# Kernel tuning notes

Measured on AMD Instinct MI355X. Metric: run time of the kernel, lower is better.

## Reference

```python
import jax, jax.numpy as jnp
import numpy as np
from jax.ops import segment_sum, segment_max

N_NODES = 100000
N_EDGES = 1600000
IN, HID, OUT = 256, 64, 40
NEG_SLOPE = 0.2  # DGL GATConv default


def setup_inputs() -> dict:
    key = jax.random.key(0)
    ks = jax.random.split(key, 12)
    feat = jax.random.normal(ks[0], (N_NODES, IN), dtype=jnp.float32)
    src = jax.random.randint(ks[1], (N_EDGES,), 0, N_NODES)
    dst = jax.random.randint(ks[2], (N_EDGES,), 0, N_NODES)
    def xavier(k, shape):
        fan = sum(shape)
        return jax.random.normal(k, shape, dtype=jnp.float32) * jnp.sqrt(2.0 / fan)
    return {
        "feat": feat, "src": src, "dst": dst,
        "W1": xavier(ks[3], (IN, HID)),  "b1": jnp.zeros((HID,), jnp.float32),
        "al1": xavier(ks[4], (HID,)),    "ar1": xavier(ks[5], (HID,)),
        "W2": xavier(ks[6], (HID, OUT)), "b2": jnp.zeros((OUT,), jnp.float32),
        "al2": xavier(ks[7], (OUT,)),    "ar2": xavier(ks[8], (OUT,)),
    }


def gat_layer(x, W, b, attn_l, attn_r, src, dst, n):
    # z: [N, F_out] projected features
    z = x @ W
    el = z @ attn_l          # [N] source attention logits
    er = z @ attn_r          # [N] destination attention logits
    e = jax.nn.leaky_relu(el[src] + er[dst], NEG_SLOPE)  # [E]
    # segment (per-destination) softmax over incoming edges
    m = segment_max(e, dst, num_segments=n)              # [N]
    w = jnp.exp(e - m[dst])                              # [E]
    s = segment_sum(w, dst, num_segments=n)              # [N]
    alpha = w / s[dst]                                   # [E]
    # scatter-add aggregation of alpha * z[src]
    out = segment_sum(alpha[:, None] * z[src], dst, num_segments=n)
    return out + b


def reference(feat, src, dst, W1, b1, al1, ar1, W2, b2, al2, ar2):
    n = feat.shape[0]
    h = gat_layer(feat, W1, b1, al1, ar1, src, dst, n)
    h = jax.nn.relu(h)  # dropout is identity in eval mode
    h = gat_layer(h, W2, b2, al2, ar2, src, dst, n)
    return jax.nn.log_softmax(h, axis=-1)  # [N, out_size]
```

## Files before the change

### kernel.cpp

```cpp
#include <hip/hip_runtime.h>
#include <math.h>

constexpr int NN   = 100000;
constexpr int NE   = 1600000;
constexpr int FIN  = 256;
constexpr int HID  = 64;
constexpr int FOUT = 40;
constexpr float SLOPE = 0.2f;
constexpr int NB    = (NN + 255) / 256;
constexpr int NBUCK = NB;
constexpr int TILE_A = 2048;
constexpr int NWG_A = (NE + TILE_A - 1) / TILE_A;
constexpr int AK = 264;

typedef short  short8  __attribute__((ext_vector_type(8)));
typedef float  floatx4 __attribute__((ext_vector_type(4)));

__device__ inline unsigned short f2bf(float x) {
    union { float f; unsigned int u; } c; c.f = x;
    unsigned int u = c.u;
    return (unsigned short)((u + 0x7FFF + ((u >> 16) & 1)) >> 16);
}

__device__ inline float readlane_f(float v, int l) {
    return __int_as_float(__builtin_amdgcn_readlane(__float_as_int(v), l));
}

__global__ __launch_bounds__(256) void w1t_kernel(
    const float* __restrict__ W1, unsigned short* __restrict__ W1T,
    const float* __restrict__ W2, const float* __restrict__ al2,
    const float* __restrict__ ar2,
    float* __restrict__ wl2, float* __restrict__ wr2)
{
    int idx = blockIdx.x * 256 + threadIdx.x;
    if (idx < FIN * HID) {
        int k = idx >> 6, n = idx & 63;
        W1T[n * FIN + k] = f2bf(W1[idx]);
    }
    if (blockIdx.x == 0 && threadIdx.x < HID) {
        int k = threadIdx.x;
        float a = 0.f, b = 0.f;
        #pragma unroll 8
        for (int j = 0; j < FOUT; ++j) {
            float wv = W2[k * FOUT + j];
            a += wv * al2[j]; b += wv * ar2[j];
        }
        wl2[k] = a; wr2[k] = b;
    }
}

__global__ __launch_bounds__(256) void gemm1_kernel(
    const float* __restrict__ feat, const unsigned short* __restrict__ W1T,
    const float* __restrict__ al, const float* __restrict__ ar,
    const int* __restrict__ dst, int* __restrict__ bcnt,
    _Float16* __restrict__ z, float* __restrict__ el, float* __restrict__ er)
{
    __shared__ unsigned short sBT[64 * AK];
    __shared__ int hist[NBUCK];
    const int t = threadIdx.x;
    const int ntile = blockIdx.x * 64;

    for (int i = t; i < NBUCK; i += 256) hist[i] = 0;
    #pragma unroll
    for (int i = 0; i < 8; ++i) {
        int g = t + 256 * i;
        int row = g >> 5, c8 = g & 31;
        *(uint4*)&sBT[row * AK + 8 * c8] = *(const uint4*)&W1T[row * FIN + 8 * c8];
    }
    __syncthreads();

    {
        int base = (blockIdx.x * 256 + t) * 4;
        if (base < NE) {
            const int4 d4 = *(const int4*)&dst[base];
            atomicAdd(&hist[d4.x >> 8], 1); atomicAdd(&hist[d4.y >> 8], 1);
            atomicAdd(&hist[d4.z >> 8], 1); atomicAdd(&hist[d4.w >> 8], 1);
        }
    }
    __syncthreads();
    for (int i = t; i < NBUCK; i += 256) {
        int hv = hist[i];
        if (hv) atomicAdd(&bcnt[i], hv);
    }

    const int w  = t >> 6;
    const int l  = t & 63;
    const int lr = l & 15;
    const int q  = l >> 4;
    const int m0 = 16 * w;

    int n = ntile + m0 + lr; if (n >= NN) n = NN - 1;
    const float* __restrict__ arow = feat + (size_t)n * FIN;

    floatx4 acc[4];
    #pragma unroll
    for (int tile = 0; tile < 4; ++tile) acc[tile] = 0.f;

    #pragma unroll
    for (int kc = 0; kc < 8; ++kc) {
        const int koff = kc * 32 + 8 * q;
        const float4 fa = *(const float4*)(arow + koff);
        const float4 fb = *(const float4*)(arow + koff + 4);
        short8 av;
        av[0] = (short)f2bf(fa.x); av[1] = (short)f2bf(fa.y);
        av[2] = (short)f2bf(fa.z); av[3] = (short)f2bf(fa.w);
        av[4] = (short)f2bf(fb.x); av[5] = (short)f2bf(fb.y);
        av[6] = (short)f2bf(fb.z); av[7] = (short)f2bf(fb.w);
        #pragma unroll
        for (int tile = 0; tile < 4; ++tile) {
            const short8 bv = *(const short8*)(sBT + (16 * tile + lr) * AK + koff);
            acc[tile] = __builtin_amdgcn_mfma_f32_16x16x32_bf16(av, bv, acc[tile], 0, 0, 0);
        }
    }

    float aln[4], arn[4];
    #pragma unroll
    for (int tile = 0; tile < 4; ++tile) {
        aln[tile] = al[16 * tile + lr];
        arn[tile] = ar[16 * tile + lr];
    }
    #pragma unroll
    for (int r = 0; r < 4; ++r) {
        int mg = ntile + m0 + 4 * q + r;
        float pl = 0.f, pr = 0.f;
        #pragma unroll
        for (int tile = 0; tile < 4; ++tile) {
            float zv = acc[tile][r];
            pl += zv * aln[tile]; pr += zv * arn[tile];
        }
        #pragma unroll
        for (int off = 8; off >= 1; off >>= 1) {
            pl += __shfl_xor(pl, off);
            pr += __shfl_xor(pr, off);
        }
        if (mg < NN) {
            #pragma unroll
            for (int tile = 0; tile < 4; ++tile)
                z[(size_t)mg * HID + 16 * tile + lr] = (_Float16)acc[tile][r];
            if (lr == 0) { el[mg] = pl; er[mg] = pr; }
        }
    }
}

__global__ __launch_bounds__(512) void scan_top_kernel(
    const int* __restrict__ bcnt, int* __restrict__ bofs, int* __restrict__ gcur)
{
    __shared__ int tmp[512];
    int t = threadIdx.x;
    int v = (t < NB) ? bcnt[t] : 0;
    tmp[t] = v; __syncthreads();
    for (int off = 1; off < 512; off <<= 1) {
        int x = (t >= off) ? tmp[t - off] : 0;
        __syncthreads();
        tmp[t] += x;
        __syncthreads();
    }
    int excl = tmp[t] - v;
    if (t < NB) { bofs[t] = excl; gcur[t] = excl; }
    if (t == NB - 1) bofs[NB] = excl + v;
}

__global__ __launch_bounds__(1024) void partitionA_kernel(
    const int* __restrict__ src, const int* __restrict__ dst,
    int* __restrict__ gcur, int* __restrict__ ebuck)
{
    __shared__ int hist[NBUCK];
    __shared__ int lcur[NBUCK];
    const int t = threadIdx.x;
    const int e0 = blockIdx.x * TILE_A;
    const int e1 = (e0 + TILE_A < NE) ? e0 + TILE_A : NE;

    for (int i = t; i < NBUCK; i += 1024) hist[i] = 0;
    __syncthreads();
    for (int e = e0 + t; e < e1; e += 1024)
        atomicAdd(&hist[dst[e] >> 8], 1);
    __syncthreads();
    for (int i = t; i < NBUCK; i += 1024) {
        int hv = hist[i];
        lcur[i] = hv ? atomicAdd(&gcur[i], hv) : 0;
    }
    __syncthreads();
    for (int e = e0 + t; e < e1; e += 1024) {
        int d = dst[e], s = src[e];
        int p = atomicAdd(&lcur[d >> 8], 1);
        ebuck[p] = (s << 8) | (d & 255);
    }
}

__global__ __launch_bounds__(1024) void partitionB_kernel(
    const int* __restrict__ bofs, const int* __restrict__ ebuck,
    int* __restrict__ row_ptr, int* __restrict__ esrc)
{
    __shared__ int sdeg[256];
    __shared__ int sscan[256];
    __shared__ int scur[256];
    const int b = blockIdx.x;
    const int n0 = b << 8;
    const int t = threadIdx.x;
    const int r0 = bofs[b], r1 = bofs[b + 1];

    if (t < 256) sdeg[t] = 0;
    __syncthreads();
    for (int e = r0 + t; e < r1; e += 1024)
        atomicAdd(&sdeg[ebuck[e] & 255], 1);
    __syncthreads();

    if (t < 256) sscan[t] = sdeg[t];
    __syncthreads();
    for (int off = 1; off < 256; off <<= 1) {
        int x = 0;
        if (t < 256 && t >= off) x = sscan[t - off];
        __syncthreads();
        if (t < 256) sscan[t] += x;
        __syncthreads();
    }
    if (t < 256) {
        int excl = sscan[t] - sdeg[t];
        if (n0 + t < NN) row_ptr[n0 + t] = r0 + excl;
        scur[t] = r0 + excl;
    }
    if (b == NBUCK - 1 && t == 0) row_ptr[NN] = NE;
    __syncthreads();

    for (int e = r0 + t; e < r1; e += 1024) {
        int pk = ebuck[e];
        int p = atomicAdd(&scur[pk & 255], 1);
        esrc[p] = pk >> 8;
    }
}

template<bool FIRST>
__global__ __launch_bounds__(256) void gat_gather_kernel(
    const int* __restrict__ row_ptr, const int* __restrict__ esrc,
    const float* __restrict__ el, const float* __restrict__ er,
    const _Float16* __restrict__ zin, const float* __restrict__ b1,
    const float* __restrict__ wl2, const float* __restrict__ wr2,
    _Float16* __restrict__ hout, float* __restrict__ haggout,
    float* __restrict__ el2, float* __restrict__ er2)
{
    const int w = threadIdx.x >> 6, lane = threadIdx.x & 63;
    const int d = blockIdx.x * 4 + w;
    const int r0 = row_ptr[d], r1 = row_ptr[d + 1];
    const int cnt = r1 - r0;
    const float erd = er[d];

    float accv = 0.f;
    float s = 0.f;

    if (cnt <= 64) {
        int sn = 0; float v = -INFINITY;
        if (lane < cnt) {
            sn = esrc[r0 + lane];
            v = el[sn] + erd;
            v = (v >= 0.f) ? v : SLOPE * v;
        }
        float m = v;
        #pragma unroll
        for (int off = 32; off >= 1; off >>= 1) m = fmaxf(m, __shfl_xor(m, off));
        float wv = (lane < cnt) ? __expf(v - m) : 0.f;
        s = wv;
        #pragma unroll
        for (int off = 32; off >= 1; off >>= 1) s += __shfl_xor(s, off);
        {
            int j = 0;
            for (; j + 8 <= cnt; j += 8) {
                float a0 = 0.f, a1 = 0.f;
                #pragma unroll
                for (int qq = 0; qq < 8; qq += 2) {
                    float w0 = readlane_f(wv, j + qq);
                    int   s0 = __builtin_amdgcn_readlane(sn, j + qq);
                    float w1 = readlane_f(wv, j + qq + 1);
                    int   s1 = __builtin_amdgcn_readlane(sn, j + qq + 1);
                    a0 += w0 * (float)zin[(size_t)s0 * HID + lane];
                    a1 += w1 * (float)zin[(size_t)s1 * HID + lane];
                }
                accv += a0 + a1;
            }
            for (; j < cnt; ++j) {
                float w0 = readlane_f(wv, j);
                int   s0 = __builtin_amdgcn_readlane(sn, j);
                accv += w0 * (float)zin[(size_t)s0 * HID + lane];
            }
        }
    } else {
        float m = -INFINITY;
        for (int e = r0 + lane; e < r1; e += 64) {
            float v = el[esrc[e]] + erd;
            v = (v >= 0.f) ? v : SLOPE * v;
            m = fmaxf(m, v);
        }
        #pragma unroll
        for (int off = 32; off >= 1; off >>= 1) m = fmaxf(m, __shfl_xor(m, off));
        for (int base = r0; base < r1; base += 64) {
            int e = base + lane;
            float wv = 0.f; int sn = 0;
            if (e < r1) {
                sn = esrc[e];
                float v = el[sn] + erd;
                v = (v >= 0.f) ? v : SLOPE * v;
                wv = __expf(v - m);
            }
            s += wv;
            int c = r1 - base; if (c > 64) c = 64;
            {
                int j = 0;
                for (; j + 4 <= c; j += 4) {
                    float a0 = 0.f, a1 = 0.f;
                    #pragma unroll
                    for (int qq = 0; qq < 4; qq += 2) {
                        float w0 = readlane_f(wv, j + qq);
                        int   s0 = __builtin_amdgcn_readlane(sn, j + qq);
                        float w1 = readlane_f(wv, j + qq + 1);
                        int   s1 = __builtin_amdgcn_readlane(sn, j + qq + 1);
                        a0 += w0 * (float)zin[(size_t)s0 * HID + lane];
                        a1 += w1 * (float)zin[(size_t)s1 * HID + lane];
                    }
                    accv += a0 + a1;
                }
                for (; j < c; ++j) {
                    float w0 = readlane_f(wv, j);
                    int   s0 = __builtin_amdgcn_readlane(sn, j);
                    accv += w0 * (float)zin[(size_t)s0 * HID + lane];
                }
            }
        }
        #pragma unroll
        for (int off = 32; off >= 1; off >>= 1) s += __shfl_xor(s, off);
    }

    float res = (cnt > 0) ? (accv / s) : 0.f;

    if (FIRST) {
        float hval = res + b1[lane];
        hval = (hval > 0.f) ? hval : 0.f;
        hout[(size_t)d * HID + lane] = (_Float16)hval;
        float pl = hval * wl2[lane];
        float pr = hval * wr2[lane];
        #pragma unroll
        for (int off = 32; off >= 1; off >>= 1) {
            pl += __shfl_xor(pl, off); pr += __shfl_xor(pr, off);
        }
        if (lane == 0) { el2[d] = pl; er2[d] = pr; }
    } else {
        haggout[(size_t)d * HID + lane] = res;
    }
}

__global__ __launch_bounds__(256) void out_kernel(
    const float* __restrict__ hagg, const float* __restrict__ W2,
    const float* __restrict__ b2, float* __restrict__ out)
{
    __shared__ float sh[4][64];
    const int w = threadIdx.x >> 6, lane = threadIdx.x & 63;
    const int n = blockIdx.x * 4 + w;
    sh[w][lane] = hagg[(size_t)n * HID + lane];
    __syncthreads();
    float acc = 0.f;
    if (lane < FOUT) {
        #pragma unroll 8
        for (int k = 0; k < HID; ++k) acc += sh[w][k] * W2[k * FOUT + lane];
    }
    float v = (lane < FOUT) ? acc + b2[lane] : -INFINITY;
    float mx = v;
    #pragma unroll
    for (int off = 32; off >= 1; off >>= 1) mx = fmaxf(mx, __shfl_xor(mx, off));
    float ex = (lane < FOUT) ? __expf(v - mx) : 0.f;
    float sm = ex;
    #pragma unroll
    for (int off = 32; off >= 1; off >>= 1) sm += __shfl_xor(sm, off);
    if (lane < FOUT) out[(size_t)n * FOUT + lane] = v - mx - __logf(sm);
}

extern "C" void kernel_launch(void* const* d_in, const int* in_sizes, int n_in,
                              void* d_out, int out_size, void* d_ws, size_t ws_size,
                              hipStream_t stream) {
    const float* feat = (const float*)d_in[0];
    const int*   src  = (const int*)d_in[1];
    const int*   dst  = (const int*)d_in[2];
    const float* W1   = (const float*)d_in[3];
    const float* b1   = (const float*)d_in[4];
    const float* al1  = (const float*)d_in[5];
    const float* ar1  = (const float*)d_in[6];
    const float* W2   = (const float*)d_in[7];
    const float* b2   = (const float*)d_in[8];
    const float* al2  = (const float*)d_in[9];
    const float* ar2  = (const float*)d_in[10];
    float* out = (float*)d_out;

    char* p = (char*)d_ws;
    float*    hagg = (float*)p;
    _Float16* z1   = (_Float16*)p;  p += (size_t)NN * HID * 4;
    _Float16* h    = (_Float16*)p;  p += (size_t)NN * HID * 2;
    float* el1   = (float*)p;     p += (size_t)NN * 4;
    float* er1   = (float*)p;     p += (size_t)NN * 4;
    float* el2   = (float*)p;     p += (size_t)NN * 4;
    float* er2   = (float*)p;     p += (size_t)NN * 4;
    float* wl2   = (float*)p;     p += HID * 4;
    float* wr2   = (float*)p;     p += HID * 4;
    int*   bcnt  = (int*)p;       p += NB * 4;
    int*   bofs  = (int*)p;       p += (NB + 1) * 4;
    int*   gcur  = (int*)p;       p += NBUCK * 4;
    int*   rowp  = (int*)p;       p += (NN + 1) * 4;
    int*   esrc  = (int*)p;       p += (size_t)NE * 4;
    int*   ebuck = (int*)p;       p += (size_t)NE * 4;
    unsigned short* w1t = (unsigned short*)p;

    hipMemsetAsync(bcnt, 0, NB * sizeof(int), stream);

    w1t_kernel<<<(FIN * HID + 255) / 256, 256, 0, stream>>>(
        W1, w1t, W2, al2, ar2, wl2, wr2);
    gemm1_kernel<<<(NN + 63) / 64, 256, 0, stream>>>(feat, w1t, al1, ar1, dst, bcnt, z1, el1, er1);

    scan_top_kernel<<<1, 512, 0, stream>>>(bcnt, bofs, gcur);
    partitionA_kernel<<<NWG_A, 1024, 0, stream>>>(src, dst, gcur, ebuck);
    partitionB_kernel<<<NBUCK, 1024, 0, stream>>>(bofs, ebuck, rowp, esrc);

    gat_gather_kernel<true><<<NN / 4, 256, 0, stream>>>(
        rowp, esrc, el1, er1, z1, b1, wl2, wr2, h, nullptr, el2, er2);

    gat_gather_kernel<false><<<NN / 4, 256, 0, stream>>>(
        rowp, esrc, el2, er2, h, nullptr, nullptr, nullptr,
        nullptr, hagg, nullptr, nullptr);

    out_kernel<<<NN / 4, 256, 0, stream>>>(hagg, W2, b2, out);
}
```

Baseline: 418.3 us.

## Merge histogram, GEMM and edge partition into fewer kernels with finer buckets

The dst-bucket histogram moves into the weight-prep kernel. The GEMM1 blocks and the partition-A blocks now share one launch, so the projection and the edge bucketing run concurrently. Each partition block recomputes the bucket prefix scan locally, which removes the standalone scan kernel. Buckets shrink from 256 to 128 nodes and the partition kernels use 256-thread blocks, trading redundant per-block scans and more buckets for fewer launches and better overlap.

Result: no change. 410.7 us (-1.8%).

```diff
diff --git a/kernel.cpp b/kernel.cpp
--- a/kernel.cpp
+++ b/kernel.cpp
@@ -7,11 +7,14 @@
 constexpr int HID  = 64;
 constexpr int FOUT = 40;
 constexpr float SLOPE = 0.2f;
-constexpr int NB    = (NN + 255) / 256;
-constexpr int NBUCK = NB;
+constexpr int NBUCK = (NN + 127) / 128;
 constexpr int TILE_A = 2048;
 constexpr int NWG_A = (NE + TILE_A - 1) / TILE_A;
+constexpr int NT_GEMM = (NN + 63) / 64;
 constexpr int AK = 264;
+constexpr int HB = 64;
+constexpr int HIST_EPB = 4096;
+constexpr int NWG_H = (NE + HIST_EPB - 1) / HIST_EPB;
 
 typedef short  short8  __attribute__((ext_vector_type(8)));
 typedef float  floatx4 __attribute__((ext_vector_type(4)));
@@ -26,195 +29,215 @@
     return __int_as_float(__builtin_amdgcn_readlane(__float_as_int(v), l));
 }
 
-__global__ __launch_bounds__(256) void w1t_kernel(
+__device__ inline void scan_buckets(const int* __restrict__ gcnt,
+                                    int* __restrict__ bofs,
+                                    int* __restrict__ tsum, int t)
+{
+    int i0 = 4 * t;
+    int c0 = (i0 + 0 < NBUCK) ? gcnt[i0 + 0] : 0;
+    int c1 = (i0 + 1 < NBUCK) ? gcnt[i0 + 1] : 0;
+    int c2 = (i0 + 2 < NBUCK) ? gcnt[i0 + 2] : 0;
+    int c3 = (i0 + 3 < NBUCK) ? gcnt[i0 + 3] : 0;
+    int s = c0 + c1 + c2 + c3;
+    tsum[t] = s;
+    __syncthreads();
+    for (int off = 1; off < 256; off <<= 1) {
+        int x = (t >= off) ? tsum[t - off] : 0;
+        __syncthreads();
+        tsum[t] += x;
+        __syncthreads();
+    }
+    int e0 = tsum[t] - s;
+    if (i0 + 0 <= NBUCK) bofs[i0 + 0] = e0;
+    if (i0 + 1 <= NBUCK) bofs[i0 + 1] = e0 + c0;
+    if (i0 + 2 <= NBUCK) bofs[i0 + 2] = e0 + c0 + c1;
+    if (i0 + 3 <= NBUCK) bofs[i0 + 3] = e0 + c0 + c1 + c2;
+    __syncthreads();
+}
+
+__global__ __launch_bounds__(256) void prep_kernel(
     const float* __restrict__ W1, unsigned short* __restrict__ W1T,
     const float* __restrict__ W2, const float* __restrict__ al2,
     const float* __restrict__ ar2,
-    float* __restrict__ wl2, float* __restrict__ wr2)
-{
-    int idx = blockIdx.x * 256 + threadIdx.x;
-    if (idx < FIN * HID) {
-        int k = idx >> 6, n = idx & 63;
-        W1T[n * FIN + k] = f2bf(W1[idx]);
-    }
-    if (blockIdx.x == 0 && threadIdx.x < HID) {
-        int k = threadIdx.x;
-        float a = 0.f, b = 0.f;
-        #pragma unroll 8
-        for (int j = 0; j < FOUT; ++j) {
-            float wv = W2[k * FOUT + j];
-            a += wv * al2[j]; b += wv * ar2[j];
-        }
-        wl2[k] = a; wr2[k] = b;
-    }
-}
-
-__global__ __launch_bounds__(256) void gemm1_kernel(
+    float* __restrict__ wl2, float* __restrict__ wr2,
+    const int* __restrict__ dst, int* __restrict__ bcnt)
+{
+    const int t = threadIdx.x;
+    if (blockIdx.x < HB) {
+        int idx = blockIdx.x * 256 + t;
+        if (idx < FIN * HID) {
+            int k = idx >> 6, n = idx & 63;
+            W1T[n * FIN + k] = f2bf(W1[idx]);
+        }
+        if (blockIdx.x == 0 && t < HID) {
+            int k = t;
+            float a = 0.f, b = 0.f;
+            #pragma unroll 8
+            for (int j = 0; j < FOUT; ++j) {
+                float wv = W2[k * FOUT + j];
+                a += wv * al2[j]; b += wv * ar2[j];
+            }
+            wl2[k] = a; wr2[k] = b;
+        }
+    } else {
+        __shared__ int hist[NBUCK];
+        for (int i = t; i < NBUCK; i += 256) hist[i] = 0;
+        __syncthreads();
+        int base = (blockIdx.x - HB) * HIST_EPB + t * 16;
+        #pragma unroll
+        for (int k = 0; k < 4; ++k) {
+            int idx = base + 4 * k;
+            if (idx < NE) {
+                const int4 d4 = *(const int4*)&dst[idx];
+                atomicAdd(&hist[d4.x >> 7], 1); atomicAdd(&hist[d4.y >> 7], 1);
+                atomicAdd(&hist[d4.z >> 7], 1); atomicAdd(&hist[d4.w >> 7], 1);
+            }
+        }
+        __syncthreads();
+        for (int i = t; i < NBUCK; i += 256) {
+            int hv = hist[i];
+            if (hv) atomicAdd(&bcnt[i], hv);
+        }
+    }
+}
+
+__global__ __launch_bounds__(256) void mega_kernel(
     const float* __restrict__ feat, const unsigned short* __restrict__ W1T,
     const float* __restrict__ al, const float* __restrict__ ar,
-    const int* __restrict__ dst, int* __restrict__ bcnt,
+    const int* __restrict__ src, const int* __restrict__ dst,
+    const int* __restrict__ bcnt, int* __restrict__ cur0,
+    int* __restrict__ ebuck,
     _Float16* __restrict__ z, float* __restrict__ el, float* __restrict__ er)
 {
-    __shared__ unsigned short sBT[64 * AK];
-    __shared__ int hist[NBUCK];
+    __shared__ int smem4[8448];
     const int t = threadIdx.x;
-    const int ntile = blockIdx.x * 64;
-
-    for (int i = t; i < NBUCK; i += 256) hist[i] = 0;
-    #pragma unroll
-    for (int i = 0; i < 8; ++i) {
-        int g = t + 256 * i;
-        int row = g >> 5, c8 = g & 31;
-        *(uint4*)&sBT[row * AK + 8 * c8] = *(const uint4*)&W1T[row * FIN + 8 * c8];
-    }
-    __syncthreads();
-
-    {
-        int base = (blockIdx.x * 256 + t) * 4;
-        if (base < NE) {
-            const int4 d4 = *(const int4*)&dst[base];
-            atomicAdd(&hist[d4.x >> 8], 1); atomicAdd(&hist[d4.y >> 8], 1);
-            atomicAdd(&hist[d4.z >> 8], 1); atomicAdd(&hist[d4.w >> 8], 1);
-        }
-    }
-    __syncthreads();
-    for (int i = t; i < NBUCK; i += 256) {
-        int hv = hist[i];
-        if (hv) atomicAdd(&bcnt[i], hv);
-    }
-
-    const int w  = t >> 6;
-    const int l  = t & 63;
-    const int lr = l & 15;
-    const int q  = l >> 4;
-    const int m0 = 16 * w;
-
-    int n = ntile + m0 + lr; if (n >= NN) n = NN - 1;
-    const float* __restrict__ arow = feat + (size_t)n * FIN;
-
-    floatx4 acc[4];
-    #pragma unroll
-    for (int tile = 0; tile < 4; ++tile) acc[tile] = 0.f;
-
-    #pragma unroll
-    for (int kc = 0; kc < 8; ++kc) {
-        const int koff = kc * 32 + 8 * q;
-        const float4 fa = *(const float4*)(arow + koff);
-        const float4 fb = *(const float4*)(arow + koff + 4);
-        short8 av;
-        av[0] = (short)f2bf(fa.x); av[1] = (short)f2bf(fa.y);
-        av[2] = (short)f2bf(fa.z); av[3] = (short)f2bf(fa.w);
-        av[4] = (short)f2bf(fb.x); av[5] = (short)f2bf(fb.y);
-        av[6] = (short)f2bf(fb.z); av[7] = (short)f2bf(fb.w);
+
+    if (blockIdx.x < NT_GEMM) {
+        unsigned short* sBT = (unsigned short*)smem4;
+        const int ntile = blockIdx.x * 64;
+
+        #pragma unroll
+        for (int i = 0; i < 8; ++i) {
+            int g = t + 256 * i;
+            int row = g >> 5, c8 = g & 31;
+            *(uint4*)&sBT[row * AK + 8 * c8] = *(const uint4*)&W1T[row * FIN + 8 * c8];
+        }
+        __syncthreads();
+
+        const int w  = t >> 6;
+        const int l  = t & 63;
+        const int lr = l & 15;
+        const int q  = l >> 4;
+        const int m0 = 16 * w;
+
+        int n = ntile + m0 + lr; if (n >= NN) n = NN - 1;
+        const float* __restrict__ arow = feat + (size_t)n * FIN;
+
+        floatx4 acc[4];
+        #pragma unroll
+        for (int tile = 0; tile < 4; ++tile) acc[tile] = 0.f;
+
+        #pragma unroll
+        for (int kc = 0; kc < 8; ++kc) {
+            const int koff = kc * 32 + 8 * q;
+            const float4 fa = *(const float4*)(arow + koff);
+            const float4 fb = *(const float4*)(arow + koff + 4);
+            short8 av;
+            av[0] = (short)f2bf(fa.x); av[1] = (short)f2bf(fa.y);
+            av[2] = (short)f2bf(fa.z); av[3] = (short)f2bf(fa.w);
+            av[4] = (short)f2bf(fb.x); av[5] = (short)f2bf(fb.y);
+            av[6] = (short)f2bf(fb.z); av[7] = (short)f2bf(fb.w);
+            #pragma unroll
+            for (int tile = 0; tile < 4; ++tile) {
+                const short8 bv = *(const short8*)(sBT + (16 * tile + lr) * AK + koff);
+                acc[tile] = __builtin_amdgcn_mfma_f32_16x16x32_bf16(av, bv, acc[tile], 0, 0, 0);
+            }
+        }
+
+        float aln[4], arn[4];
         #pragma unroll
         for (int tile = 0; tile < 4; ++tile) {
-            const short8 bv = *(const short8*)(sBT + (16 * tile + lr) * AK + koff);
-            acc[tile] = __builtin_amdgcn_mfma_f32_16x16x32_bf16(av, bv, acc[tile], 0, 0, 0);
-        }
-    }
-
-    float aln[4], arn[4];
-    #pragma unroll
-    for (int tile = 0; tile < 4; ++tile) {
-        aln[tile] = al[16 * tile + lr];
-        arn[tile] = ar[16 * tile + lr];
-    }
-    #pragma unroll
-    for (int r = 0; r < 4; ++r) {
-        int mg = ntile + m0 + 4 * q + r;
-        float pl = 0.f, pr = 0.f;
-        #pragma unroll
-        for (int tile = 0; tile < 4; ++tile) {
-            float zv = acc[tile][r];
-            pl += zv * aln[tile]; pr += zv * arn[tile];
-        }
-        #pragma unroll
-        for (int off = 8; off >= 1; off >>= 1) {
-            pl += __shfl_xor(pl, off);
-            pr += __shfl_xor(pr, off);
-        }
-        if (mg < NN) {
+            aln[tile] = al[16 * tile + lr];
+            arn[tile] = ar[16 * tile + lr];
+        }
+        #pragma unroll
+        for (int r = 0; r < 4; ++r) {
+            int mg = ntile + m0 + 4 * q + r;
+            float pl = 0.f, pr = 0.f;
             #pragma unroll
-            for (int tile = 0; tile < 4; ++tile)
-                z[(size_t)mg * HID + 16 * tile + lr] = (_Float16)acc[tile][r];
-            if (lr == 0) { el[mg] = pl; er[mg] = pr; }
-        }
-    }
-}
-
-__global__ __launch_bounds__(512) void scan_top_kernel(
-    const int* __restrict__ bcnt, int* __restrict__ bofs, int* __restrict__ gcur)
-{
-    __shared__ int tmp[512];
-    int t = threadIdx.x;
-    int v = (t < NB) ? bcnt[t] : 0;
-    tmp[t] = v; __syncthreads();
-    for (int off = 1; off < 512; off <<= 1) {
-        int x = (t >= off) ? tmp[t - off] : 0;
-        __syncthreads();
-        tmp[t] += x;
-        __syncthreads();
-    }
-    int excl = tmp[t] - v;
-    if (t < NB) { bofs[t] = excl; gcur[t] = excl; }
-    if (t == NB - 1) bofs[NB] = excl + v;
-}
-
-__global__ __launch_bounds__(1024) void partitionA_kernel(
-    const int* __restrict__ src, const int* __restrict__ dst,
-    int* __restrict__ gcur, int* __restrict__ ebuck)
-{
-    __shared__ int hist[NBUCK];
-    __shared__ int lcur[NBUCK];
+            for (int tile = 0; tile < 4; ++tile) {
+                float zv = acc[tile][r];
+                pl += zv * aln[tile]; pr += zv * arn[tile];
+            }
+            #pragma unroll
+            for (int off = 8; off >= 1; off >>= 1) {
+                pl += __shfl_xor(pl, off);
+                pr += __shfl_xor(pr, off);
+            }
+            if (mg < NN) {
+                #pragma unroll
+                for (int tile = 0; tile < 4; ++tile)
+                    z[(size_t)mg * HID + 16 * tile + lr] = (_Float16)acc[tile][r];
+                if (lr == 0) { el[mg] = pl; er[mg] = pr; }
+            }
+        }
+    } else {
+        int* hist = smem4;
+        int* bofs = smem4 + NBUCK;
+        int* tsum = smem4 + 2 * NBUCK + 1;
+        int* lcur = smem4 + 2 * NBUCK + 1 + 256;
+        const int blk = blockIdx.x - NT_GEMM;
+        const int e0 = blk * TILE_A;
+        const int e1 = (e0 + TILE_A < NE) ? e0 + TILE_A : NE;
+
+        for (int i = t; i < NBUCK; i += 256) hist[i] = 0;
+        scan_buckets(bcnt, bofs, tsum, t);
+        for (int e = e0 + t; e < e1; e += 256)
+            atomicAdd(&hist[dst[e] >> 7], 1);
+        __syncthreads();
+        for (int i = t; i < NBUCK; i += 256) {
+            int hv = hist[i];
+            if (hv) lcur[i] = bofs[i] + atomicAdd(&cur0[i], hv);
+        }
+        __syncthreads();
+        for (int e = e0 + t; e < e1; e += 256) {
+            int d = dst[e], s_ = src[e];
+            int p = atomicAdd(&lcur[d >> 7], 1);
+            ebuck[p] = (s_ << 7) | (d & 127);
+        }
+    }
+}
+
+__global__ __launch_bounds__(256) void partB_kernel(
+    const int* __restrict__ bcnt, const int* __restrict__ ebuck,
+    int* __restrict__ row_ptr, int* __restrict__ esrc)
+{
+    __shared__ int bofs[NBUCK + 1];
+    __shared__ int tsum[256];
+    __shared__ int sdeg[128];
+    __shared__ int sscan[128];
+    __shared__ int scur[128];
+    const int b = blockIdx.x;
+    const int n0 = b << 7;
     const int t = threadIdx.x;
-    const int e0 = blockIdx.x * TILE_A;
-    const int e1 = (e0 + TILE_A < NE) ? e0 + TILE_A : NE;
-
-    for (int i = t; i < NBUCK; i += 1024) hist[i] = 0;
-    __syncthreads();
-    for (int e = e0 + t; e < e1; e += 1024)
-        atomicAdd(&hist[dst[e] >> 8], 1);
-    __syncthreads();
-    for (int i = t; i < NBUCK; i += 1024) {
-        int hv = hist[i];
-        lcur[i] = hv ? atomicAdd(&gcur[i], hv) : 0;
-    }
-    __syncthreads();
-    for (int e = e0 + t; e < e1; e += 1024) {
-        int d = dst[e], s = src[e];
-        int p = atomicAdd(&lcur[d >> 8], 1);
-        ebuck[p] = (s << 8) | (d & 255);
-    }
-}
-
-__global__ __launch_bounds__(1024) void partitionB_kernel(
-    const int* __restrict__ bofs, const int* __restrict__ ebuck,
-    int* __restrict__ row_ptr, int* __restrict__ esrc)
-{
-    __shared__ int sdeg[256];
-    __shared__ int sscan[256];
-    __shared__ int scur[256];
-    const int b = blockIdx.x;
-    const int n0 = b << 8;
-    const int t = threadIdx.x;
+
+    if (t < 128) sdeg[t] = 0;
+    scan_buckets(bcnt, bofs, tsum, t);
     const int r0 = bofs[b], r1 = bofs[b + 1];
 
-    if (t < 256) sdeg[t] = 0;
-    __syncthreads();
-    for (int e = r0 + t; e < r1; e += 1024)
-        atomicAdd(&sdeg[ebuck[e] & 255], 1);
-    __syncthreads();
-
-    if (t < 256) sscan[t] = sdeg[t];
-    __syncthreads();
-    for (int off = 1; off < 256; off <<= 1) {
-        int x = 0;
-        if (t < 256 && t >= off) x = sscan[t - off];
-        __syncthreads();
-        if (t < 256) sscan[t] += x;
-        __syncthreads();
-    }
-    if (t < 256) {
+    for (int e = r0 + t; e < r1; e += 256)
+        atomicAdd(&sdeg[ebuck[e] & 127], 1);
+    __syncthreads();
+
+    if (t < 128) sscan[t] = sdeg[t];
+    __syncthreads();
+    for (int off = 1; off < 128; off <<= 1) {
+        int x = (t < 128 && t >= off) ? sscan[t - off] : 0;
+        __syncthreads();
+        if (t < 128) sscan[t] += x;
+        __syncthreads();
+    }
+    if (t < 128) {
         int excl = sscan[t] - sdeg[t];
         if (n0 + t < NN) row_ptr[n0 + t] = r0 + excl;
         scur[t] = r0 + excl;
@@ -222,10 +245,10 @@
     if (b == NBUCK - 1 && t == 0) row_ptr[NN] = NE;
     __syncthreads();
 
-    for (int e = r0 + t; e < r1; e += 1024) {
+    for (int e = r0 + t; e < r1; e += 256) {
         int pk = ebuck[e];
-        int p = atomicAdd(&scur[pk & 255], 1);
-        esrc[p] = pk >> 8;
+        int p = atomicAdd(&scur[pk & 127], 1);
+        esrc[p] = pk >> 7;
     }
 }
 
@@ -397,23 +420,22 @@
     float* er2   = (float*)p;     p += (size_t)NN * 4;
     float* wl2   = (float*)p;     p += HID * 4;
     float* wr2   = (float*)p;     p += HID * 4;
-    int*   bcnt  = (int*)p;       p += NB * 4;
-    int*   bofs  = (int*)p;       p += (NB + 1) * 4;
-    int*   gcur  = (int*)p;       p += NBUCK * 4;
+    int*   bcnt  = (int*)p;       p += NBUCK * 4;
+    int*   cur0  = (int*)p;       p += NBUCK * 4;
     int*   rowp  = (int*)p;       p += (NN + 1) * 4;
     int*   esrc  = (int*)p;       p += (size_t)NE * 4;
     int*   ebuck = (int*)p;       p += (size_t)NE * 4;
     unsigned short* w1t = (unsigned short*)p;
 
-    hipMemsetAsync(bcnt, 0, NB * sizeof(int), stream);
-
-    w1t_kernel<<<(FIN * HID + 255) / 256, 256, 0, stream>>>(
-        W1, w1t, W2, al2, ar2, wl2, wr2);
-    gemm1_kernel<<<(NN + 63) / 64, 256, 0, stream>>>(feat, w1t, al1, ar1, dst, bcnt, z1, el1, er1);
-
-    scan_top_kernel<<<1, 512, 0, stream>>>(bcnt, bofs, gcur);
-    partitionA_kernel<<<NWG_A, 1024, 0, stream>>>(src, dst, gcur, ebuck);
-    partitionB_kernel<<<NBUCK, 1024, 0, stream>>>(bofs, ebuck, rowp, esrc);
+    hipMemsetAsync(bcnt, 0, 2 * NBUCK * sizeof(int), stream);
+
+    prep_kernel<<<HB + NWG_H, 256, 0, stream>>>(
+        W1, w1t, W2, al2, ar2, wl2, wr2, dst, bcnt);
+
+    mega_kernel<<<NT_GEMM + NWG_A, 256, 0, stream>>>(
+        feat, w1t, al1, ar1, src, dst, bcnt, cur0, ebuck, z1, el1, er1);
+
+    partB_kernel<<<NBUCK, 256, 0, stream>>>(bcnt, ebuck, rowp, esrc);
 
     gat_gather_kernel<true><<<NN / 4, 256, 0, stream>>>(
         rowp, esrc, el1, er1, z1, b1, wl2, wr2, h, nullptr, el2, er2);
```
